# Performance work log

Measured on AMD Instinct MI355X. Metric: run time of the kernel, lower is better.

Reference implementation:

```python
import jax, jax.numpy as jnp
import numpy as np
import math

D = 128       # d_model (file-scope constant)
L_LEN = 128   # length; forced == d_model by the un-transposed attention call
NH = 4        # n_head
DK = D // NH
K = 7         # depthwise conv kernel size
LC = 4        # conv_num
EPS = 1e-5    # LayerNorm eps
NEG = -1e30


def _pos_encoding():
    i = np.arange(D).astype(np.float64)
    freqs = np.where(i % 2 == 0, 10000.0 ** (-i / D), -(10000.0 ** ((1 - i) / D)))
    phases = np.where(i % 2 == 0, 0.0, math.pi / 2)
    pos = np.arange(L_LEN).astype(np.float64)[None, :]          # (1, L)
    pe = np.sin(pos * freqs[:, None] + phases[:, None])          # (D, L)
    return jnp.asarray(pe, jnp.float32)

PE = _pos_encoding()


def layernorm2d(x, w, b):
    # LayerNorm over the trailing (D, L) dims jointly, elementwise affine (D, L)
    mu = x.mean(axis=(-2, -1), keepdims=True)
    var = x.var(axis=(-2, -1), keepdims=True)
    return (x - mu) * jax.lax.rsqrt(var + EPS) * w + b


def sep_conv(x, dw_w, dw_b, pw_w, pw_b):
    # depthwise conv1d (groups=C) then 1x1 pointwise conv. x: (B, C, L)
    h = jax.lax.conv_general_dilated(
        x, dw_w[:, None, :], window_strides=(1,), padding=[(K // 2, K // 2)],
        dimension_numbers=('NCH', 'OIH', 'NCH'), feature_group_count=D)
    h = h + dw_b[:, None]
    return jnp.einsum('bcl,oc->bol', h, pw_w) + pw_b[:, None]


def mha(x, mask_f, Wq, bq, Wk, bk, Wv, bv, Wo, bo):
    # x: (B, Lx, F) with Lx == F == D here (module feeds (B, d_model, length) untransposed)
    B, Lx, _ = x.shape
    q = (x @ Wq.T + bq).reshape(B, Lx, NH, DK)
    k = (x @ Wk.T + bk).reshape(B, Lx, NH, DK)
    v = (x @ Wv.T + bv).reshape(B, Lx, NH, DK)
    scores = jnp.einsum('bqhd,bkhd->bhqk', q, k) * (1.0 / math.sqrt(DK))
    m = mask_f[:, None, None, :]                         # (B,1,1,Lx)
    scores = scores * (1.0 - m) + m * NEG                # mask_logits
    attn = jax.nn.softmax(scores, axis=-1)
    out = jnp.einsum('bhqk,bkhd->bqhd', attn, v).reshape(B, Lx, D)
    return out @ Wo.T + bo


def setup_inputs() -> dict:
    key = jax.random.key(0)
    ks = jax.random.split(key, 16)
    B = 1024
    s = 0.02
    inp = {
        'x': jax.random.normal(ks[0], (B, D, L_LEN), jnp.float32),
        'mask': jax.random.randint(ks[1], (B, L_LEN), 0, 2, jnp.int32),
        'dw_w': jax.random.normal(ks[2], (LC, D, K), jnp.float32) * s,
        'dw_b': jnp.zeros((LC, D), jnp.float32),
        'pw_w': jax.random.normal(ks[3], (LC, D, D), jnp.float32) * s,
        'pw_b': jnp.zeros((LC, D), jnp.float32),
        'normb_w': jnp.ones((D, L_LEN), jnp.float32),
        'normb_b': jnp.zeros((D, L_LEN), jnp.float32),
        'norms_w': jnp.ones((LC, D, L_LEN), jnp.float32),
        'norms_b': jnp.zeros((LC, D, L_LEN), jnp.float32),
        'norme_w': jnp.ones((D, L_LEN), jnp.float32),
        'norme_b': jnp.zeros((D, L_LEN), jnp.float32),
        'Wq': jax.random.normal(ks[4], (D, D), jnp.float32) * s,
        'bq': jnp.zeros((D,), jnp.float32),
        'Wk': jax.random.normal(ks[5], (D, D), jnp.float32) * s,
        'bk': jnp.zeros((D,), jnp.float32),
        'Wv': jax.random.normal(ks[6], (D, D), jnp.float32) * s,
        'bv': jnp.zeros((D,), jnp.float32),
        'Wo': jax.random.normal(ks[7], (D, D), jnp.float32) * s,
        'bo': jnp.zeros((D,), jnp.float32),
        'fc_w': jax.random.normal(ks[8], (D, D), jnp.float32) * s,
        'fc_b': jnp.zeros((D,), jnp.float32),
    }
    return inp


def reference(x, mask, dw_w, dw_b, pw_w, pw_b, normb_w, normb_b, norms_w, norms_b,
              norme_w, norme_b, Wq, bq, Wk, bk, Wv, bv, Wo, bo, fc_w, fc_b):
    # Eval mode: all dropouts are identity.
    mask_f = mask.astype(x.dtype)
    out = x + PE                                  # PosEncoder
    res = out
    out = layernorm2d(out, normb_w, normb_b)      # normb
    for i in range(LC):                           # fixed small layer loop
        h = sep_conv(out, dw_w[i], dw_b[i], pw_w[i], pw_b[i])
        out = jax.nn.relu(h) + res
        res = out
        out = layernorm2d(out, norms_w[i], norms_b[i])
    att = mha(out, mask_f, Wq, bq, Wk, bk, Wv, bv, Wo, bo)
    out = att + res
    res = out
    out = layernorm2d(out, norme_w, norme_b)
    # fc applied over channel dim: (B,C,L)->(B,L,C) linear ->(B,C,L)
    h = jnp.einsum('bcl,oc->bol', out, fc_w) + fc_b[:, None]
    out = jax.nn.relu(h) + res
    return out
```

## Files before the change

### kernel.cpp

```cpp
#include <hip/hip_runtime.h>

#define NEGF -1e30f
#define EPSF 1e-5f

typedef __attribute__((ext_vector_type(8))) short bf16x8;
typedef __attribute__((ext_vector_type(4))) float f32x4;

#define WSU_PW 0
#define WSU_FC 65536
#define WSU_WO 81920
#define WSU_WQ 98304
#define WSU_WK 114688
#define WSU_WV 131072
#define WSU_END 147456

__device__ __forceinline__ unsigned short f2bf(float x) {
  unsigned int u = __float_as_uint(x);
  u += 0x7fffu + ((u >> 16) & 1u);
  return (unsigned short)(u >> 16);
}
__device__ __forceinline__ float bf2f(unsigned short u) {
  return __uint_as_float(((unsigned int)u) << 16);
}
__device__ __forceinline__ f32x4 mfma16(bf16x8 a, bf16x8 b, f32x4 c) {
  return __builtin_amdgcn_mfma_f32_16x16x32_bf16(a, b, c, 0, 0, 0);
}

__global__ __launch_bounds__(128) void prep_kernel(
    const float* __restrict__ pw_w, const float* __restrict__ fc_w,
    const float* __restrict__ Wo, const float* __restrict__ Wq,
    const float* __restrict__ Wk, const float* __restrict__ Wv,
    unsigned short* __restrict__ wsu) {
  int job = blockIdx.x, r = blockIdx.y, c = threadIdx.x;
  int idx = r * 128 + c;
  if (job < 4)       wsu[WSU_PW + job * 16384 + idx] = f2bf(pw_w[job * 16384 + idx]);
  else if (job == 4) wsu[WSU_FC + idx] = f2bf(fc_w[idx]);
  else if (job == 5) wsu[WSU_WO + idx] = f2bf(Wo[idx]);
  else if (job == 6) wsu[WSU_WQ + idx] = f2bf(Wq[idx]);
  else if (job == 7) wsu[WSU_WK + idx] = f2bf(Wk[idx]);
  else if (job == 8) wsu[WSU_WV + idx] = f2bf(Wv[idx]);
  else {
    float* pe = (float*)(wsu + WSU_END);
    int d = r, pos = c;
    double freq, phase;
    if ((d & 1) == 0) { freq = pow(10000.0, -(double)d / 128.0); phase = 0.0; }
    else { freq = -pow(10000.0, (1.0 - (double)d) / 128.0); phase = 1.5707963267948966; }
    pe[d * 128 + pos] = (float)sin((double)pos * freq + phase);
  }
}

__device__ __forceinline__ void ln_stats(const float* resv, float* red, int t,
                                         float& mu, float& inv) {
  float s = 0.f, s2 = 0.f;
#pragma unroll
  for (int i = 0; i < 32; i++) { float v = resv[i]; s += v; s2 += v * v; }
#pragma unroll
  for (int off = 32; off > 0; off >>= 1) {
    s += __shfl_down(s, off, 64);
    s2 += __shfl_down(s2, off, 64);
  }
  if ((t & 63) == 0) { red[(t >> 6) * 2] = s; red[(t >> 6) * 2 + 1] = s2; }
  __syncthreads();
  float S = 0.f, S2 = 0.f;
#pragma unroll
  for (int i = 0; i < 8; i++) { S += red[2 * i]; S2 += red[2 * i + 1]; }
  mu = S * (1.0f / 16384.0f);
  float var = S2 * (1.0f / 16384.0f) - mu * mu;
  inv = rsqrtf(var + EPSF);
}

__global__ __launch_bounds__(512, 1) void enc_kernel(
    const float* __restrict__ x, const int* __restrict__ mask,
    const float* __restrict__ dw_w, const float* __restrict__ dw_b,
    const float* __restrict__ pw_b,
    const float* __restrict__ normb_w, const float* __restrict__ normb_b,
    const float* __restrict__ norms_w, const float* __restrict__ norms_b,
    const float* __restrict__ norme_w, const float* __restrict__ norme_b,
    const float* __restrict__ bq, const float* __restrict__ bk,
    const float* __restrict__ bv, const float* __restrict__ bo,
    const float* __restrict__ fc_b, const unsigned short* __restrict__ wsu,
    const float* __restrict__ pe, float* __restrict__ out) {
  __shared__ __align__(16) float S[128 * 130];
  __shared__ __align__(16) unsigned short Xn_raw[128 * 136 + 16];
  __shared__ __align__(16) unsigned short HT[128 * 136];
  __shared__ float mask_s[128];
  __shared__ float red[16];
  unsigned short* Xn = Xn_raw + 8;
  unsigned short* Pn  = (unsigned short*)S;
  unsigned short* Qh  = Pn + 128 * 136;
  unsigned short* Kh  = Qh + 128 * 40;
  unsigned short* VTh = Kh + 128 * 40;

  const int t = threadIdx.x;
  const int b = blockIdx.x;
  const int lane = t & 63;
  const int r16 = lane & 15;
  const int quad = lane >> 4;
  const int m0 = __builtin_amdgcn_readfirstlane((t >> 6) << 4);
  const int l = t & 127;
  const int obase = __builtin_amdgcn_readfirstlane((t >> 7) << 5);
  const int dw_o = t & 127;
  const int dw_seg = __builtin_amdgcn_readfirstlane(t >> 7);

  if (t < 128) mask_s[t] = (float)mask[b * 128 + t];

  float res[32];
  {
    const float* xb = x + (size_t)b * 16384;
#pragma unroll
    for (int i = 0; i < 32; i++) {
      int o = obase + i;
      res[i] = xb[o * 128 + l] + pe[o * 128 + l];
    }
  }
  {
    float mu, inv;
    ln_stats(res, red, t, mu, inv);
#pragma unroll
    for (int i = 0; i < 32; i++) {
      int o = obase + i;
      Xn[o * 136 + l] = f2bf((res[i] - mu) * inv * normb_w[o * 128 + l] + normb_b[o * 128 + l]);
    }
    __syncthreads();
  }

#pragma unroll 1
  for (int layer = 0; layer < 4; layer++) {
    {
      const float* dwp = dw_w + layer * 896 + dw_o * 7;
      float wreg[7];
#pragma unroll
      for (int j = 0; j < 7; j++) wreg[j] = dwp[j];
      float bias = dw_b[layer * 128 + dw_o];
      const unsigned short* xrow = Xn + dw_o * 136 + dw_seg * 32 - 8;
      float f[48];
#pragma unroll
      for (int i6 = 0; i6 < 6; i6++) {
        bf16x8 v = *(const bf16x8*)(xrow + 8 * i6);
#pragma unroll
        for (int j = 0; j < 8; j++) f[i6 * 8 + j] = bf2f((unsigned short)v[j]);
      }
      if (dw_seg == 0) {
#pragma unroll
        for (int i = 0; i < 8; i++) f[i] = 0.f;
      }
      if (dw_seg == 3) {
#pragma unroll
        for (int i = 40; i < 48; i++) f[i] = 0.f;
      }
      float accv[32];
#pragma unroll
      for (int c = 0; c < 32; c++) {
        float a = bias;
#pragma unroll
        for (int j = 0; j < 7; j++) a += f[c + 5 + j] * wreg[j];
        accv[c] = a;
      }
#pragma unroll
      for (int c = 0; c < 32; c++) HT[(dw_seg * 32 + c) * 136 + dw_o] = f2bf(accv[c]);
    }
    __syncthreads();
    {
      const unsigned short* pwp = wsu + WSU_PW + (layer << 14) + (m0 + r16) * 128 + quad * 8;
      bf16x8 a0 = *(const bf16x8*)(pwp);
      bf16x8 a1 = *(const bf16x8*)(pwp + 32);
      bf16x8 a2 = *(const bf16x8*)(pwp + 64);
      bf16x8 a3 = *(const bf16x8*)(pwp + 96);
#pragma unroll
      for (int n = 0; n < 8; n++) {
        const unsigned short* hb = HT + (16 * n + r16) * 136 + quad * 8;
        f32x4 c = {0.f, 0.f, 0.f, 0.f};
        c = mfma16(a0, *(const bf16x8*)(hb), c);
        c = mfma16(a1, *(const bf16x8*)(hb + 32), c);
        c = mfma16(a2, *(const bf16x8*)(hb + 64), c);
        c = mfma16(a3, *(const bf16x8*)(hb + 96), c);
        float* sp = S + (m0 + quad * 4) * 130 + 16 * n + r16;
        sp[0] = c[0]; sp[130] = c[1]; sp[260] = c[2]; sp[390] = c[3];
      }
    }
    __syncthreads();
    {
#pragma unroll
      for (int i = 0; i < 32; i++)
        res[i] += fmaxf(S[(obase + i) * 130 + l] + pw_b[layer * 128 + obase + i], 0.f);
      float mu, inv;
      ln_stats(res, red, t, mu, inv);
      const float* wg = norms_w + layer * 16384;
      const float* bg = norms_b + layer * 16384;
#pragma unroll
      for (int i = 0; i < 32; i++) {
        int o = obase + i;
        Xn[o * 136 + l] = f2bf((res[i] - mu) * inv * wg[o * 128 + l] + bg[o * 128 + l]);
      }
      __syncthreads();
    }
  }

#pragma unroll 1
  for (int h = 0; h < 4; h++) {
    __syncthreads();
    {
      const unsigned short* xp = Xn + (m0 + r16) * 136 + quad * 8;
      bf16x8 x0 = *(const bf16x8*)(xp);
      bf16x8 x1 = *(const bf16x8*)(xp + 32);
      bf16x8 x2 = *(const bf16x8*)(xp + 64);
      bf16x8 x3 = *(const bf16x8*)(xp + 96);
#pragma unroll
      for (int n = 0; n < 2; n++) {
        const int jrow = 32 * h + 16 * n + r16;
        {
          const unsigned short* wp = wsu + WSU_WQ + jrow * 128 + quad * 8;
          f32x4 c = {0.f, 0.f, 0.f, 0.f};
          c = mfma16(x0, *(const bf16x8*)(wp), c);
          c = mfma16(x1, *(const bf16x8*)(wp + 32), c);
          c = mfma16(x2, *(const bf16x8*)(wp + 64), c);
          c = mfma16(x3, *(const bf16x8*)(wp + 96), c);
          float bb = bq[jrow];
#pragma unroll
          for (int r = 0; r < 4; r++)
            Qh[(m0 + quad * 4 + r) * 40 + 16 * n + r16] =
                f2bf((c[r] + bb) * 0.17677669529663687f);
        }
        {
          const unsigned short* wp = wsu + WSU_WK + jrow * 128 + quad * 8;
          f32x4 c = {0.f, 0.f, 0.f, 0.f};
          c = mfma16(x0, *(const bf16x8*)(wp), c);
          c = mfma16(x1, *(const bf16x8*)(wp + 32), c);
          c = mfma16(x2, *(const bf16x8*)(wp + 64), c);
          c = mfma16(x3, *(const bf16x8*)(wp + 96), c);
          float bb = bk[jrow];
#pragma unroll
          for (int r = 0; r < 4; r++)
            Kh[(m0 + quad * 4 + r) * 40 + 16 * n + r16] = f2bf(c[r] + bb);
        }
        {
          const unsigned short* wp = wsu + WSU_WV + jrow * 128 + quad * 8;
          f32x4 c = {0.f, 0.f, 0.f, 0.f};
          c = mfma16(x0, *(const bf16x8*)(wp), c);
          c = mfma16(x1, *(const bf16x8*)(wp + 32), c);
          c = mfma16(x2, *(const bf16x8*)(wp + 64), c);
          c = mfma16(x3, *(const bf16x8*)(wp + 96), c);
          float bb = bv[jrow];
          unsigned int lo = (unsigned int)f2bf(c[0] + bb) | ((unsigned int)f2bf(c[1] + bb) << 16);
          unsigned int hi = (unsigned int)f2bf(c[2] + bb) | ((unsigned int)f2bf(c[3] + bb) << 16);
          unsigned short* vp = VTh + (16 * n + r16) * 136 + m0 + quad * 4;
          *(unsigned int*)(vp) = lo;
          *(unsigned int*)(vp + 2) = hi;
        }
      }
    }
    __syncthreads();
    float linv[4];
    {
      bf16x8 aq = *(const bf16x8*)(Qh + (m0 + r16) * 40 + quad * 8);
      f32x4 sc[8];
#pragma unroll
      for (int n = 0; n < 8; n++) {
        f32x4 z = {0.f, 0.f, 0.f, 0.f};
        sc[n] = mfma16(aq, *(const bf16x8*)(Kh + (16 * n + r16) * 40 + quad * 8), z);
      }
      float mv[8];
#pragma unroll
      for (int n = 0; n < 8; n++) mv[n] = mask_s[16 * n + r16];
#pragma unroll
      for (int r = 0; r < 4; r++) {
        float sv[8];
#pragma unroll
        for (int n = 0; n < 8; n++) sv[n] = (mv[n] > 0.5f) ? NEGF : sc[n][r];
        float mx = sv[0];
#pragma unroll
        for (int n = 1; n < 8; n++) mx = fmaxf(mx, sv[n]);
        mx = fmaxf(mx, __shfl_xor(mx, 1, 64));
        mx = fmaxf(mx, __shfl_xor(mx, 2, 64));
        mx = fmaxf(mx, __shfl_xor(mx, 4, 64));
        mx = fmaxf(mx, __shfl_xor(mx, 8, 64));
        float sum = 0.f;
#pragma unroll
        for (int n = 0; n < 8; n++) { float p = __expf(sv[n] - mx); sv[n] = p; sum += p; }
        sum += __shfl_xor(sum, 1, 64);
        sum += __shfl_xor(sum, 2, 64);
        sum += __shfl_xor(sum, 4, 64);
        sum += __shfl_xor(sum, 8, 64);
        linv[r] = 1.0f / sum;
        unsigned short* pp = Pn + (m0 + quad * 4 + r) * 136 + r16;
#pragma unroll
        for (int n = 0; n < 8; n++) pp[16 * n] = f2bf(sv[n]);
      }
    }
    {
      const unsigned short* pq = Pn + (m0 + r16) * 136 + quad * 8;
      bf16x8 p0 = *(const bf16x8*)(pq);
      bf16x8 p1 = *(const bf16x8*)(pq + 32);
      bf16x8 p2 = *(const bf16x8*)(pq + 64);
      bf16x8 p3 = *(const bf16x8*)(pq + 96);
#pragma unroll
      for (int n = 0; n < 2; n++) {
        const unsigned short* vb = VTh + (16 * n + r16) * 136 + quad * 8;
        f32x4 c = {0.f, 0.f, 0.f, 0.f};
        c = mfma16(p0, *(const bf16x8*)(vb), c);
        c = mfma16(p1, *(const bf16x8*)(vb + 32), c);
        c = mfma16(p2, *(const bf16x8*)(vb + 64), c);
        c = mfma16(p3, *(const bf16x8*)(vb + 96), c);
#pragma unroll
        for (int r = 0; r < 4; r++)
          HT[(m0 + quad * 4 + r) * 136 + 32 * h + 16 * n + r16] = f2bf(c[r] * linv[r]);
      }
    }
  }
  __syncthreads();

  {
    const unsigned short* ap = HT + (m0 + r16) * 136 + quad * 8;
    bf16x8 a0 = *(const bf16x8*)(ap);
    bf16x8 a1 = *(const bf16x8*)(ap + 32);
    bf16x8 a2 = *(const bf16x8*)(ap + 64);
    bf16x8 a3 = *(const bf16x8*)(ap + 96);
#pragma unroll
    for (int n = 0; n < 8; n++) {
      const unsigned short* wp = wsu + WSU_WO + (16 * n + r16) * 128 + quad * 8;
      f32x4 c = {0.f, 0.f, 0.f, 0.f};
      c = mfma16(a0, *(const bf16x8*)(wp), c);
      c = mfma16(a1, *(const bf16x8*)(wp + 32), c);
      c = mfma16(a2, *(const bf16x8*)(wp + 64), c);
      c = mfma16(a3, *(const bf16x8*)(wp + 96), c);
      float* sp = S + (m0 + quad * 4) * 130 + 16 * n + r16;
      sp[0] = c[0]; sp[130] = c[1]; sp[260] = c[2]; sp[390] = c[3];
    }
  }
  __syncthreads();
  {
    float bol = bo[l];
#pragma unroll
    for (int i = 0; i < 32; i++) res[i] += S[(obase + i) * 130 + l] + bol;
    float mu, inv;
    ln_stats(res, red, t, mu, inv);
#pragma unroll
    for (int i = 0; i < 32; i += 2) {
      int o = obase + i;
      float v0 = (res[i] - mu) * inv * norme_w[o * 128 + l] + norme_b[o * 128 + l];
      float v1 = (res[i + 1] - mu) * inv * norme_w[(o + 1) * 128 + l] + norme_b[(o + 1) * 128 + l];
      *(unsigned int*)(HT + l * 136 + o) =
          (unsigned int)f2bf(v0) | ((unsigned int)f2bf(v1) << 16);
    }
    __syncthreads();
  }
  {
    const unsigned short* fp = wsu + WSU_FC + (m0 + r16) * 128 + quad * 8;
    bf16x8 a0 = *(const bf16x8*)(fp);
    bf16x8 a1 = *(const bf16x8*)(fp + 32);
    bf16x8 a2 = *(const bf16x8*)(fp + 64);
    bf16x8 a3 = *(const bf16x8*)(fp + 96);
#pragma unroll
    for (int n = 0; n < 8; n++) {
      const unsigned short* hb = HT + (16 * n + r16) * 136 + quad * 8;
      f32x4 c = {0.f, 0.f, 0.f, 0.f};
      c = mfma16(a0, *(const bf16x8*)(hb), c);
      c = mfma16(a1, *(const bf16x8*)(hb + 32), c);
      c = mfma16(a2, *(const bf16x8*)(hb + 64), c);
      c = mfma16(a3, *(const bf16x8*)(hb + 96), c);
      float* sp = S + (m0 + quad * 4) * 130 + 16 * n + r16;
      sp[0] = c[0]; sp[130] = c[1]; sp[260] = c[2]; sp[390] = c[3];
    }
  }
  __syncthreads();
  {
    float* outb = out + (size_t)b * 16384;
#pragma unroll
    for (int i = 0; i < 32; i++) {
      float hv = S[(obase + i) * 130 + l] + fc_b[obase + i];
      outb[(obase + i) * 128 + l] = fmaxf(hv, 0.f) + res[i];
    }
  }
}

extern "C" void kernel_launch(void* const* d_in, const int* in_sizes, int n_in,
                              void* d_out, int out_size, void* d_ws, size_t ws_size,
                              hipStream_t stream) {
  const float* x       = (const float*)d_in[0];
  const int*   mask    = (const int*)d_in[1];
  const float* dw_w    = (const float*)d_in[2];
  const float* dw_b    = (const float*)d_in[3];
  const float* pw_w    = (const float*)d_in[4];
  const float* pw_b    = (const float*)d_in[5];
  const float* normb_w = (const float*)d_in[6];
  const float* normb_b = (const float*)d_in[7];
  const float* norms_w = (const float*)d_in[8];
  const float* norms_b = (const float*)d_in[9];
  const float* norme_w = (const float*)d_in[10];
  const float* norme_b = (const float*)d_in[11];
  const float* Wq      = (const float*)d_in[12];
  const float* bq      = (const float*)d_in[13];
  const float* Wk      = (const float*)d_in[14];
  const float* bk      = (const float*)d_in[15];
  const float* Wv      = (const float*)d_in[16];
  const float* bv      = (const float*)d_in[17];
  const float* Wo      = (const float*)d_in[18];
  const float* bo      = (const float*)d_in[19];
  const float* fc_w    = (const float*)d_in[20];
  const float* fc_b    = (const float*)d_in[21];
  float* out = (float*)d_out;
  unsigned short* wsu = (unsigned short*)d_ws;
  const float* pe = (const float*)(wsu + WSU_END);
  int B = in_sizes[0] / 16384;

  prep_kernel<<<dim3(10, 128), dim3(128), 0, stream>>>(pw_w, fc_w, Wo, Wq, Wk, Wv, wsu);
  enc_kernel<<<dim3(B), dim3(512), 0, stream>>>(
      x, mask, dw_w, dw_b, pw_b, normb_w, normb_b, norms_w, norms_b,
      norme_w, norme_b, bq, bk, bv, bo, fc_b, wsu, pe, out);
}
```

Measured before the change: 612.9 us.

## Shrink LDS footprint with bf16 intermediates to fit multiple blocks per CU

Removes the fp32 staging buffer and stores GEMM outputs as bf16 in two shared ping-pong buffers, which roughly halves LDS use so more than one 512-thread block can reside per CU. Launch bounds rise to request 4 blocks. The depthwise conv is rewritten to work in 8-wide chunks with fewer live registers. Attention probabilities go through a half-width P buffer in two phases, and per-head outputs are kept in registers. The costs are lower precision on the pointwise, Wo and fc outputs, and likely register spills under the tighter VGPR budget.

```diff
diff --git a/kernel.cpp b/kernel.cpp
--- a/kernel.cpp
+++ b/kernel.cpp
@@ -5,6 +5,8 @@
 
 typedef __attribute__((ext_vector_type(8))) short bf16x8;
 typedef __attribute__((ext_vector_type(4))) float f32x4;
+typedef unsigned short u16;
+typedef unsigned int u32;
 
 #define WSU_PW 0
 #define WSU_FC 65536
@@ -14,13 +16,13 @@
 #define WSU_WV 131072
 #define WSU_END 147456
 
-__device__ __forceinline__ unsigned short f2bf(float x) {
-  unsigned int u = __float_as_uint(x);
+__device__ __forceinline__ u16 f2bf(float x) {
+  u32 u = __float_as_uint(x);
   u += 0x7fffu + ((u >> 16) & 1u);
-  return (unsigned short)(u >> 16);
-}
-__device__ __forceinline__ float bf2f(unsigned short u) {
-  return __uint_as_float(((unsigned int)u) << 16);
+  return (u16)(u >> 16);
+}
+__device__ __forceinline__ float bf2f(u16 u) {
+  return __uint_as_float(((u32)u) << 16);
 }
 __device__ __forceinline__ f32x4 mfma16(bf16x8 a, bf16x8 b, f32x4 c) {
   return __builtin_amdgcn_mfma_f32_16x16x32_bf16(a, b, c, 0, 0, 0);
@@ -30,7 +32,7 @@
     const float* __restrict__ pw_w, const float* __restrict__ fc_w,
     const float* __restrict__ Wo, const float* __restrict__ Wq,
     const float* __restrict__ Wk, const float* __restrict__ Wv,
-    unsigned short* __restrict__ wsu) {
+    u16* __restrict__ wsu) {
   int job = blockIdx.x, r = blockIdx.y, c = threadIdx.x;
   int idx = r * 128 + c;
   if (job < 4)       wsu[WSU_PW + job * 16384 + idx] = f2bf(pw_w[job * 16384 + idx]);
@@ -69,7 +71,7 @@
   inv = rsqrtf(var + EPSF);
 }
 
-__global__ __launch_bounds__(512, 1) void enc_kernel(
+__global__ __launch_bounds__(512, 4) void enc_kernel(
     const float* __restrict__ x, const int* __restrict__ mask,
     const float* __restrict__ dw_w, const float* __restrict__ dw_b,
     const float* __restrict__ pw_b,
@@ -78,18 +80,17 @@
     const float* __restrict__ norme_w, const float* __restrict__ norme_b,
     const float* __restrict__ bq, const float* __restrict__ bk,
     const float* __restrict__ bv, const float* __restrict__ bo,
-    const float* __restrict__ fc_b, const unsigned short* __restrict__ wsu,
+    const float* __restrict__ fc_b, const u16* __restrict__ wsu,
     const float* __restrict__ pe, float* __restrict__ out) {
-  __shared__ __align__(16) float S[128 * 130];
-  __shared__ __align__(16) unsigned short Xn_raw[128 * 136 + 16];
-  __shared__ __align__(16) unsigned short HT[128 * 136];
+  __shared__ __align__(16) u16 A_raw[128 * 136 + 16];
+  __shared__ __align__(16) u16 B_[128 * 136];
   __shared__ float mask_s[128];
   __shared__ float red[16];
-  unsigned short* Xn = Xn_raw + 8;
-  unsigned short* Pn  = (unsigned short*)S;
-  unsigned short* Qh  = Pn + 128 * 136;
-  unsigned short* Kh  = Qh + 128 * 40;
-  unsigned short* VTh = Kh + 128 * 40;
+  u16* A = A_raw + 8;
+  u16* QH = B_;
+  u16* KH = B_ + 5120;
+  u16* VT = B_ + 10240;
+  u16* PN = B_;
 
   const int t = threadIdx.x;
   const int b = blockIdx.x;
@@ -119,7 +120,7 @@
 #pragma unroll
     for (int i = 0; i < 32; i++) {
       int o = obase + i;
-      Xn[o * 136 + l] = f2bf((res[i] - mu) * inv * normb_w[o * 128 + l] + normb_b[o * 128 + l]);
+      A[o * 136 + l] = f2bf((res[i] - mu) * inv * normb_w[o * 128 + l] + normb_b[o * 128 + l]);
     }
     __syncthreads();
   }
@@ -132,57 +133,52 @@
 #pragma unroll
       for (int j = 0; j < 7; j++) wreg[j] = dwp[j];
       float bias = dw_b[layer * 128 + dw_o];
-      const unsigned short* xrow = Xn + dw_o * 136 + dw_seg * 32 - 8;
-      float f[48];
-#pragma unroll
-      for (int i6 = 0; i6 < 6; i6++) {
-        bf16x8 v = *(const bf16x8*)(xrow + 8 * i6);
-#pragma unroll
-        for (int j = 0; j < 8; j++) f[i6 * 8 + j] = bf2f((unsigned short)v[j]);
-      }
-      if (dw_seg == 0) {
-#pragma unroll
-        for (int i = 0; i < 8; i++) f[i] = 0.f;
-      }
-      if (dw_seg == 3) {
-#pragma unroll
-        for (int i = 40; i < 48; i++) f[i] = 0.f;
-      }
-      float accv[32];
-#pragma unroll
-      for (int c = 0; c < 32; c++) {
-        float a = bias;
-#pragma unroll
-        for (int j = 0; j < 7; j++) a += f[c + 5 + j] * wreg[j];
-        accv[c] = a;
-      }
-#pragma unroll
-      for (int c = 0; c < 32; c++) HT[(dw_seg * 32 + c) * 136 + dw_o] = f2bf(accv[c]);
-    }
-    __syncthreads();
-    {
-      const unsigned short* pwp = wsu + WSU_PW + (layer << 14) + (m0 + r16) * 128 + quad * 8;
+      const u16* xrow = A + dw_o * 136;
+#pragma unroll
+      for (int k = 0; k < 4; k++) {
+        const int lb = dw_seg * 32 + 8 * k;
+        bf16x8 vz = {0, 0, 0, 0, 0, 0, 0, 0};
+        bf16x8 vc = *(const bf16x8*)(xrow + lb);
+        bf16x8 vp = (dw_seg == 0 && k == 0) ? vz : *(const bf16x8*)(xrow + lb - 8);
+        bf16x8 vn = (dw_seg == 3 && k == 3) ? vz : *(const bf16x8*)(xrow + lb + 8);
+        float w14[14];
+        w14[0] = bf2f((u16)vp[5]); w14[1] = bf2f((u16)vp[6]); w14[2] = bf2f((u16)vp[7]);
+#pragma unroll
+        for (int j = 0; j < 8; j++) w14[3 + j] = bf2f((u16)vc[j]);
+        w14[11] = bf2f((u16)vn[0]); w14[12] = bf2f((u16)vn[1]); w14[13] = bf2f((u16)vn[2]);
+#pragma unroll
+        for (int j = 0; j < 8; j++) {
+          float a = bias;
+#pragma unroll
+          for (int tt = 0; tt < 7; tt++) a += w14[j + tt] * wreg[tt];
+          B_[(lb + j) * 136 + dw_o] = f2bf(a);
+        }
+      }
+    }
+    __syncthreads();
+    {
+      const u16* pwp = wsu + WSU_PW + (layer << 14) + (m0 + r16) * 128 + quad * 8;
       bf16x8 a0 = *(const bf16x8*)(pwp);
       bf16x8 a1 = *(const bf16x8*)(pwp + 32);
       bf16x8 a2 = *(const bf16x8*)(pwp + 64);
       bf16x8 a3 = *(const bf16x8*)(pwp + 96);
 #pragma unroll
       for (int n = 0; n < 8; n++) {
-        const unsigned short* hb = HT + (16 * n + r16) * 136 + quad * 8;
+        const u16* hb = B_ + (16 * n + r16) * 136 + quad * 8;
         f32x4 c = {0.f, 0.f, 0.f, 0.f};
         c = mfma16(a0, *(const bf16x8*)(hb), c);
         c = mfma16(a1, *(const bf16x8*)(hb + 32), c);
         c = mfma16(a2, *(const bf16x8*)(hb + 64), c);
         c = mfma16(a3, *(const bf16x8*)(hb + 96), c);
-        float* sp = S + (m0 + quad * 4) * 130 + 16 * n + r16;
-        sp[0] = c[0]; sp[130] = c[1]; sp[260] = c[2]; sp[390] = c[3];
+        u16* sp = A + (m0 + quad * 4) * 136 + 16 * n + r16;
+        sp[0] = f2bf(c[0]); sp[136] = f2bf(c[1]); sp[272] = f2bf(c[2]); sp[408] = f2bf(c[3]);
       }
     }
     __syncthreads();
     {
 #pragma unroll
       for (int i = 0; i < 32; i++)
-        res[i] += fmaxf(S[(obase + i) * 130 + l] + pw_b[layer * 128 + obase + i], 0.f);
+        res[i] += fmaxf(bf2f(A[(obase + i) * 136 + l]) + pw_b[layer * 128 + obase + i], 0.f);
       float mu, inv;
       ln_stats(res, red, t, mu, inv);
       const float* wg = norms_w + layer * 16384;
@@ -190,17 +186,17 @@
 #pragma unroll
       for (int i = 0; i < 32; i++) {
         int o = obase + i;
-        Xn[o * 136 + l] = f2bf((res[i] - mu) * inv * wg[o * 128 + l] + bg[o * 128 + l]);
+        A[o * 136 + l] = f2bf((res[i] - mu) * inv * wg[o * 128 + l] + bg[o * 128 + l]);
       }
       __syncthreads();
     }
   }
 
-#pragma unroll 1
+  float att[32];
+#pragma unroll
   for (int h = 0; h < 4; h++) {
-    __syncthreads();
-    {
-      const unsigned short* xp = Xn + (m0 + r16) * 136 + quad * 8;
+    {
+      const u16* xp = A + (m0 + r16) * 136 + quad * 8;
       bf16x8 x0 = *(const bf16x8*)(xp);
       bf16x8 x1 = *(const bf16x8*)(xp + 32);
       bf16x8 x2 = *(const bf16x8*)(xp + 64);
@@ -209,7 +205,7 @@
       for (int n = 0; n < 2; n++) {
         const int jrow = 32 * h + 16 * n + r16;
         {
-          const unsigned short* wp = wsu + WSU_WQ + jrow * 128 + quad * 8;
+          const u16* wp = wsu + WSU_WQ + jrow * 128 + quad * 8;
           f32x4 c = {0.f, 0.f, 0.f, 0.f};
           c = mfma16(x0, *(const bf16x8*)(wp), c);
           c = mfma16(x1, *(const bf16x8*)(wp + 32), c);
@@ -218,11 +214,11 @@
           float bb = bq[jrow];
 #pragma unroll
           for (int r = 0; r < 4; r++)
-            Qh[(m0 + quad * 4 + r) * 40 + 16 * n + r16] =
+            QH[(m0 + quad * 4 + r) * 40 + 16 * n + r16] =
                 f2bf((c[r] + bb) * 0.17677669529663687f);
         }
         {
-          const unsigned short* wp = wsu + WSU_WK + jrow * 128 + quad * 8;
+          const u16* wp = wsu + WSU_WK + jrow * 128 + quad * 8;
           f32x4 c = {0.f, 0.f, 0.f, 0.f};
           c = mfma16(x0, *(const bf16x8*)(wp), c);
           c = mfma16(x1, *(const bf16x8*)(wp + 32), c);
@@ -231,34 +227,38 @@
           float bb = bk[jrow];
 #pragma unroll
           for (int r = 0; r < 4; r++)
-            Kh[(m0 + quad * 4 + r) * 40 + 16 * n + r16] = f2bf(c[r] + bb);
+            KH[(m0 + quad * 4 + r) * 40 + 16 * n + r16] = f2bf(c[r] + bb);
         }
         {
-          const unsigned short* wp = wsu + WSU_WV + jrow * 128 + quad * 8;
+          const u16* wp = wsu + WSU_WV + jrow * 128 + quad * 8;
           f32x4 c = {0.f, 0.f, 0.f, 0.f};
           c = mfma16(x0, *(const bf16x8*)(wp), c);
           c = mfma16(x1, *(const bf16x8*)(wp + 32), c);
           c = mfma16(x2, *(const bf16x8*)(wp + 64), c);
           c = mfma16(x3, *(const bf16x8*)(wp + 96), c);
           float bb = bv[jrow];
-          unsigned int lo = (unsigned int)f2bf(c[0] + bb) | ((unsigned int)f2bf(c[1] + bb) << 16);
-          unsigned int hi = (unsigned int)f2bf(c[2] + bb) | ((unsigned int)f2bf(c[3] + bb) << 16);
-          unsigned short* vp = VTh + (16 * n + r16) * 136 + m0 + quad * 4;
-          *(unsigned int*)(vp) = lo;
-          *(unsigned int*)(vp + 2) = hi;
+          u32 lo = (u32)f2bf(c[0] + bb) | ((u32)f2bf(c[1] + bb) << 16);
+          u32 hi = (u32)f2bf(c[2] + bb) | ((u32)f2bf(c[3] + bb) << 16);
+          u16* vp = VT + (16 * n + r16) * 136 + m0 + quad * 4;
+          *(u32*)(vp) = lo;
+          *(u32*)(vp + 2) = hi;
         }
       }
     }
     __syncthreads();
-    float linv[4];
-    {
-      bf16x8 aq = *(const bf16x8*)(Qh + (m0 + r16) * 40 + quad * 8);
-      f32x4 sc[8];
+    f32x4 sc[8];
+    {
+      bf16x8 aq = *(const bf16x8*)(QH + (m0 + r16) * 40 + quad * 8);
 #pragma unroll
       for (int n = 0; n < 8; n++) {
         f32x4 z = {0.f, 0.f, 0.f, 0.f};
-        sc[n] = mfma16(aq, *(const bf16x8*)(Kh + (16 * n + r16) * 40 + quad * 8), z);
-      }
+        sc[n] = mfma16(aq, *(const bf16x8*)(KH + (16 * n + r16) * 40 + quad * 8), z);
+      }
+    }
+    __syncthreads();
+    float linv[4];
+    u32 pk2[8];
+    {
       float mv[8];
 #pragma unroll
       for (int n = 0; n < 8; n++) mv[n] = mask_s[16 * n + r16];
@@ -282,56 +282,76 @@
         sum += __shfl_xor(sum, 4, 64);
         sum += __shfl_xor(sum, 8, 64);
         linv[r] = 1.0f / sum;
-        unsigned short* pp = Pn + (m0 + quad * 4 + r) * 136 + r16;
-#pragma unroll
-        for (int n = 0; n < 8; n++) pp[16 * n] = f2bf(sv[n]);
-      }
-    }
-    {
-      const unsigned short* pq = Pn + (m0 + r16) * 136 + quad * 8;
+        u16* pp = PN + (m0 + quad * 4 + r) * 72 + r16;
+        pp[0] = f2bf(sv[0]); pp[16] = f2bf(sv[1]);
+        pp[32] = f2bf(sv[2]); pp[48] = f2bf(sv[3]);
+        pk2[r * 2 + 0] = (u32)f2bf(sv[4]) | ((u32)f2bf(sv[5]) << 16);
+        pk2[r * 2 + 1] = (u32)f2bf(sv[6]) | ((u32)f2bf(sv[7]) << 16);
+      }
+    }
+    f32x4 pv0 = {0.f, 0.f, 0.f, 0.f}, pv1 = {0.f, 0.f, 0.f, 0.f};
+    {
+      const u16* pq = PN + (m0 + r16) * 72 + quad * 8;
       bf16x8 p0 = *(const bf16x8*)(pq);
       bf16x8 p1 = *(const bf16x8*)(pq + 32);
-      bf16x8 p2 = *(const bf16x8*)(pq + 64);
-      bf16x8 p3 = *(const bf16x8*)(pq + 96);
-#pragma unroll
-      for (int n = 0; n < 2; n++) {
-        const unsigned short* vb = VTh + (16 * n + r16) * 136 + quad * 8;
-        f32x4 c = {0.f, 0.f, 0.f, 0.f};
-        c = mfma16(p0, *(const bf16x8*)(vb), c);
-        c = mfma16(p1, *(const bf16x8*)(vb + 32), c);
-        c = mfma16(p2, *(const bf16x8*)(vb + 64), c);
-        c = mfma16(p3, *(const bf16x8*)(vb + 96), c);
-#pragma unroll
-        for (int r = 0; r < 4; r++)
-          HT[(m0 + quad * 4 + r) * 136 + 32 * h + 16 * n + r16] = f2bf(c[r] * linv[r]);
-      }
-    }
-  }
-  __syncthreads();
-
-  {
-    const unsigned short* ap = HT + (m0 + r16) * 136 + quad * 8;
+      const u16* vb0 = VT + r16 * 136 + quad * 8;
+      const u16* vb1 = VT + (16 + r16) * 136 + quad * 8;
+      pv0 = mfma16(p0, *(const bf16x8*)(vb0), pv0);
+      pv0 = mfma16(p1, *(const bf16x8*)(vb0 + 32), pv0);
+      pv1 = mfma16(p0, *(const bf16x8*)(vb1), pv1);
+      pv1 = mfma16(p1, *(const bf16x8*)(vb1 + 32), pv1);
+#pragma unroll
+      for (int r = 0; r < 4; r++) {
+        u16* pp = PN + (m0 + quad * 4 + r) * 72 + r16;
+        pp[0] = (u16)pk2[r * 2 + 0]; pp[16] = (u16)(pk2[r * 2 + 0] >> 16);
+        pp[32] = (u16)pk2[r * 2 + 1]; pp[48] = (u16)(pk2[r * 2 + 1] >> 16);
+      }
+      bf16x8 p2 = *(const bf16x8*)(pq);
+      bf16x8 p3 = *(const bf16x8*)(pq + 32);
+      pv0 = mfma16(p2, *(const bf16x8*)(vb0 + 64), pv0);
+      pv0 = mfma16(p3, *(const bf16x8*)(vb0 + 96), pv0);
+      pv1 = mfma16(p2, *(const bf16x8*)(vb1 + 64), pv1);
+      pv1 = mfma16(p3, *(const bf16x8*)(vb1 + 96), pv1);
+    }
+#pragma unroll
+    for (int r = 0; r < 4; r++) {
+      att[h * 8 + r] = pv0[r] * linv[r];
+      att[h * 8 + 4 + r] = pv1[r] * linv[r];
+    }
+    __syncthreads();
+  }
+
+#pragma unroll
+  for (int h = 0; h < 4; h++)
+#pragma unroll
+    for (int np = 0; np < 2; np++)
+#pragma unroll
+      for (int r = 0; r < 4; r++)
+        A[(m0 + quad * 4 + r) * 136 + 32 * h + 16 * np + r16] =
+            f2bf(att[h * 8 + np * 4 + r]);
+  {
+    const u16* ap = A + (m0 + r16) * 136 + quad * 8;
     bf16x8 a0 = *(const bf16x8*)(ap);
     bf16x8 a1 = *(const bf16x8*)(ap + 32);
     bf16x8 a2 = *(const bf16x8*)(ap + 64);
     bf16x8 a3 = *(const bf16x8*)(ap + 96);
 #pragma unroll
     for (int n = 0; n < 8; n++) {
-      const unsigned short* wp = wsu + WSU_WO + (16 * n + r16) * 128 + quad * 8;
+      const u16* wp = wsu + WSU_WO + (16 * n + r16) * 128 + quad * 8;
       f32x4 c = {0.f, 0.f, 0.f, 0.f};
       c = mfma16(a0, *(const bf16x8*)(wp), c);
       c = mfma16(a1, *(const bf16x8*)(wp + 32), c);
       c = mfma16(a2, *(const bf16x8*)(wp + 64), c);
       c = mfma16(a3, *(const bf16x8*)(wp + 96), c);
-      float* sp = S + (m0 + quad * 4) * 130 + 16 * n + r16;
-      sp[0] = c[0]; sp[130] = c[1]; sp[260] = c[2]; sp[390] = c[3];
+      u16* sp = B_ + (m0 + quad * 4) * 136 + 16 * n + r16;
+      sp[0] = f2bf(c[0]); sp[136] = f2bf(c[1]); sp[272] = f2bf(c[2]); sp[408] = f2bf(c[3]);
     }
   }
   __syncthreads();
   {
     float bol = bo[l];
 #pragma unroll
-    for (int i = 0; i < 32; i++) res[i] += S[(obase + i) * 130 + l] + bol;
+    for (int i = 0; i < 32; i++) res[i] += bf2f(B_[(obase + i) * 136 + l]) + bol;
     float mu, inv;
     ln_stats(res, red, t, mu, inv);
 #pragma unroll
@@ -339,27 +359,26 @@
       int o = obase + i;
       float v0 = (res[i] - mu) * inv * norme_w[o * 128 + l] + norme_b[o * 128 + l];
       float v1 = (res[i + 1] - mu) * inv * norme_w[(o + 1) * 128 + l] + norme_b[(o + 1) * 128 + l];
-      *(unsigned int*)(HT + l * 136 + o) =
-          (unsigned int)f2bf(v0) | ((unsigned int)f2bf(v1) << 16);
-    }
-    __syncthreads();
-  }
-  {
-    const unsigned short* fp = wsu + WSU_FC + (m0 + r16) * 128 + quad * 8;
+      *(u32*)(A + l * 136 + o) = (u32)f2bf(v0) | ((u32)f2bf(v1) << 16);
+    }
+    __syncthreads();
+  }
+  {
+    const u16* fp = wsu + WSU_FC + (m0 + r16) * 128 + quad * 8;
     bf16x8 a0 = *(const bf16x8*)(fp);
     bf16x8 a1 = *(const bf16x8*)(fp + 32);
     bf16x8 a2 = *(const bf16x8*)(fp + 64);
     bf16x8 a3 = *(const bf16x8*)(fp + 96);
 #pragma unroll
     for (int n = 0; n < 8; n++) {
-      const unsigned short* hb = HT + (16 * n + r16) * 136 + quad * 8;
+      const u16* hb = A + (16 * n + r16) * 136 + quad * 8;
       f32x4 c = {0.f, 0.f, 0.f, 0.f};
       c = mfma16(a0, *(const bf16x8*)(hb), c);
       c = mfma16(a1, *(const bf16x8*)(hb + 32), c);
       c = mfma16(a2, *(const bf16x8*)(hb + 64), c);
       c = mfma16(a3, *(const bf16x8*)(hb + 96), c);
-      float* sp = S + (m0 + quad * 4) * 130 + 16 * n + r16;
-      sp[0] = c[0]; sp[130] = c[1]; sp[260] = c[2]; sp[390] = c[3];
+      u16* sp = B_ + (m0 + quad * 4) * 136 + 16 * n + r16;
+      sp[0] = f2bf(c[0]); sp[136] = f2bf(c[1]); sp[272] = f2bf(c[2]); sp[408] = f2bf(c[3]);
     }
   }
   __syncthreads();
@@ -367,7 +386,7 @@
     float* outb = out + (size_t)b * 16384;
 #pragma unroll
     for (int i = 0; i < 32; i++) {
-      float hv = S[(obase + i) * 130 + l] + fc_b[obase + i];
+      float hv = bf2f(B_[(obase + i) * 136 + l]) + fc_b[obase + i];
       outb[(obase + i) * 128 + l] = fmaxf(hv, 0.f) + res[i];
     }
   }
@@ -399,7 +418,7 @@
   const float* fc_w    = (const float*)d_in[20];
   const float* fc_b    = (const float*)d_in[21];
   float* out = (float*)d_out;
-  unsigned short* wsu = (unsigned short*)d_ws;
+  u16* wsu = (u16*)d_ws;
   const float* pe = (const float*)(wsu + WSU_END);
   int B = in_sizes[0] / 16384;
 
```

New measurement: 678.2 us. 10.7% more time.
